# Kernel optimization log

Measured on AMD Instinct MI355X. Metric: run time of the kernel, lower is better.

Reference implementation:

```python
import jax, jax.numpy as jnp
import numpy as np

CHUNK = 64

def _l2norm(x, eps=1e-6):
    return x * jax.lax.rsqrt(jnp.sum(x * x, axis=-1, keepdims=True) + eps)

def _gated_delta_rule(query, key, value, g, beta, chunk_size=CHUNK):
    """Chunked gated delta-rule linear attention (Qwen3.5 GatedDeltaNet).
    query/key: [B,S,H,Dk], value: [B,S,H,Dv], g/beta: [B,S,H]. Returns [B,S,H,Dv]."""
    out_dtype = query.dtype
    # use_qk_l2norm_in_kernel=True
    query = _l2norm(query)
    key = _l2norm(key)
    # -> [B,H,S,D] fp32 (matches torch kernel's internal fp32 math)
    q, k, v = [jnp.transpose(x, (0, 2, 1, 3)).astype(jnp.float32) for x in (query, key, value)]
    gg, b = [jnp.transpose(x, (0, 2, 1)).astype(jnp.float32) for x in (g, beta)]
    B, H, S, Dk = k.shape
    Dv = v.shape[-1]
    C = chunk_size
    pad = (-S) % C  # static
    if pad:
        q = jnp.pad(q, ((0, 0), (0, 0), (0, pad), (0, 0)))
        k = jnp.pad(k, ((0, 0), (0, 0), (0, pad), (0, 0)))
        v = jnp.pad(v, ((0, 0), (0, 0), (0, pad), (0, 0)))
        gg = jnp.pad(gg, ((0, 0), (0, 0), (0, pad)))
        b = jnp.pad(b, ((0, 0), (0, 0), (0, pad)))
    Tlen = S + pad
    N = Tlen // C
    q = q * (Dk ** -0.5)
    v_beta = v * b[..., None]
    k_beta = k * b[..., None]
    rs = lambda x: x.reshape(B, H, N, C, x.shape[-1])
    q, k, v_beta, k_beta = map(rs, (q, k, v_beta, k_beta))
    gc = jnp.cumsum(gg.reshape(B, H, N, C), axis=-1)  # within-chunk cumulative log-decay
    tril = jnp.tril(jnp.ones((C, C), bool))
    strict = jnp.tril(jnp.ones((C, C), bool), -1)
    diff = gc[..., :, None] - gc[..., None, :]  # [B,H,N,C,C]
    decay = jnp.where(tril, jnp.exp(jnp.where(tril, diff, 0.0)), 0.0)
    # UT transform: torch's sequential row loop computes (I + strict_tril(k_beta k^T * decay))^{-1}
    M = jnp.where(strict, jnp.einsum('bhnck,bhndk->bhncd', k_beta, k) * decay, 0.0)
    eye = jnp.eye(C, dtype=jnp.float32)
    Tmat = jax.scipy.linalg.solve_triangular(eye + M, jnp.broadcast_to(eye, M.shape), lower=True)
    v_c = Tmat @ v_beta                                   # [B,H,N,C,Dv]
    k_cum = Tmat @ (k_beta * jnp.exp(gc)[..., None])      # [B,H,N,C,Dk]

    def step(state, inp):
        q_i, k_i, v_i, kc_i, dec_i, g_i = inp  # per-chunk [B,H,C,*]
        attn = jnp.einsum('bhck,bhdk->bhcd', q_i, k_i) * dec_i
        v_new = v_i - kc_i @ state
        out_i = (q_i * jnp.exp(g_i)[..., None]) @ state + attn @ v_new
        g_last = g_i[..., -1]
        kd = k_i * jnp.exp(g_last[..., None] - g_i)[..., None]
        state = state * jnp.exp(g_last)[..., None, None] + jnp.einsum('bhck,bhcv->bhkv', kd, v_new)
        return state, out_i

    mv = lambda x: jnp.moveaxis(x, 2, 0)  # chunk axis leading for scan
    init = jnp.zeros((B, H, Dk, Dv), jnp.float32)
    _, outs = jax.lax.scan(step, init, (mv(q), mv(k), mv(v_c), mv(k_cum), mv(decay), mv(gc)))
    out = jnp.moveaxis(outs, 0, 2).reshape(B, H, Tlen, Dv)[:, :, :S]
    return jnp.transpose(out, (0, 2, 1, 3)).astype(out_dtype)


def setup_inputs() -> dict:
    key = jax.random.key(0)
    ks = jax.random.split(key, 5)
    B, S, H, Dk, Dv = 2, 4096, 16, 128, 128
    q = jax.random.normal(ks[0], (B, S, H, Dk), jnp.float32)
    k = jax.random.normal(ks[1], (B, S, H, Dk), jnp.float32)
    v = jax.random.normal(ks[2], (B, S, H, Dv), jnp.float32)
    # g is log-decay, <= 0 (model computes g = -exp(A_log)*softplus(a + dt_bias))
    g = -jax.random.uniform(ks[3], (B, S, H), jnp.float32)
    beta = jax.random.uniform(ks[4], (B, S, H), jnp.float32)  # ~ sigmoid(b)
    return {"query": q, "key": k, "value": v, "g": g, "beta": beta}


def reference(query, key, value, g, beta):
    return _gated_delta_rule(query, key, value, g, beta)
```

## Files before the change

kernel.cpp:

```cpp
#include <hip/hip_runtime.h>
#include <math.h>


namespace {
constexpr int Bn = 2, Sn = 4096, Hn = 16, DKn = 128, DVn = 128, Cn = 64, Nn = 64;
constexpr int NBH = 32;
constexpr long CHUNK_B = 143360;
}

typedef __attribute__((ext_vector_type(4))) float f32x4;
typedef __attribute__((ext_vector_type(8))) _Float16 f16x8;
typedef __attribute__((ext_vector_type(4))) _Float16 f16x4;

__device__ __forceinline__ void fsplit(float x, _Float16& h, _Float16& l) {
  h = (_Float16)x;
  l = (_Float16)(x - (float)h);
}

__device__ __forceinline__ void gl_lds16(const void* g, void* l) {
  __builtin_amdgcn_global_load_lds(
      (const __attribute__((address_space(1))) void*)g,
      (__attribute__((address_space(3))) void*)l, 16, 0, 0);
}

#define MFMA16(D, A, B) D = __builtin_amdgcn_mfma_f32_16x16x32_f16(A, B, D, 0, 0, 0)

__device__ __forceinline__ int sidx(int r, int dk) {
  return r * 128 + (((dk >> 3) ^ (r & 7)) << 3) + (dk & 7);
}

__global__ __launch_bounds__(512, 1) void gdn_phaseA(
    const float* __restrict__ q, const float* __restrict__ k,
    const float* __restrict__ v, const float* __restrict__ g,
    const float* __restrict__ beta, char* __restrict__ wsb,
    int n0, int ncpp)
{
  __shared__ __align__(16) _Float16 sAh[8192], sAl[8192];
  __shared__ __align__(16) _Float16 sQh[8192], sQl[8192];
  __shared__ __align__(16) float sM[64][68];
  __shared__ __align__(16) float satt[4096];
  __shared__ __align__(16) float sV[64 * 132];
  __shared__ float s_gc[64], s_egc[64], s_inv[64], s_ekd[64], s_beta[64];

  const int t    = threadIdx.x;
  const int lane = t & 63;
  const int w    = t >> 6;
  const int pl  = blockIdx.x;
  const int bhx = pl / ncpp;
  const int nl  = pl % ncpp;
  const int n   = n0 + nl;
  const int hh_ = bhx % Hn;
  const int bb_ = bhx / Hn;
  const long base   = (((long)bb_ * Sn + (long)n * Cn) * Hn + hh_) * DKn;
  const long rowstr = (long)Hn * DKn;
  const long gbase  = ((long)bb_ * Sn + (long)n * Cn) * Hn + hh_;
  const long cb     = (long)pl * CHUNK_B;
  const long gloff  = (long)NBH * ncpp * CHUNK_B;

  #pragma unroll
  for (int i = 0; i < 4; ++i) {
    int idx = t + 512 * i;
    int r = idx >> 5, c4 = (idx & 31) << 2;
    *(f32x4*)&sV[r * 132 + c4] = *(const f32x4*)(v + base + (long)r * rowstr + c4);
  }

  if (t < 64) {
    s_beta[t] = beta[gbase + (long)t * Hn];
    float x = g[gbase + (long)t * Hn];
    #pragma unroll
    for (int s = 1; s < 64; s <<= 1) {
      float y = __shfl_up(x, s, 64);
      if (t >= s) x += y;
    }
    s_gc[t]  = x;
    float eg = expf(x);
    s_egc[t] = eg;
    s_inv[t] = expf(-x);
    float g63 = __shfl(x, 63, 64);
    s_ekd[t] = expf(g63 - x);
    if (t == 63) ((float*)(wsb + gloff))[pl] = eg;
  }

  {
    const int r = t >> 3, sub = t & 7;
    f32x4 ka[4], qa[4];
    #pragma unroll
    for (int i = 0; i < 4; ++i) {
      ka[i] = *(const f32x4*)(k + base + (long)r * rowstr + sub * 16 + 4 * i);
      qa[i] = *(const f32x4*)(q + base + (long)r * rowstr + sub * 16 + 4 * i);
    }
    float sk = 0.f, sq = 0.f;
    #pragma unroll
    for (int i = 0; i < 4; ++i) {
      sk += ka[i][0]*ka[i][0] + ka[i][1]*ka[i][1] + ka[i][2]*ka[i][2] + ka[i][3]*ka[i][3];
      sq += qa[i][0]*qa[i][0] + qa[i][1]*qa[i][1] + qa[i][2]*qa[i][2] + qa[i][3]*qa[i][3];
    }
    sk += __shfl_xor(sk, 1, 64); sk += __shfl_xor(sk, 2, 64); sk += __shfl_xor(sk, 4, 64);
    sq += __shfl_xor(sq, 1, 64); sq += __shfl_xor(sq, 2, 64); sq += __shfl_xor(sq, 4, 64);
    const float rk = rsqrtf(sk + 1e-6f);
    const float rq = rsqrtf(sq + 1e-6f) * 0.08838834764831845f;
    #pragma unroll
    for (int i = 0; i < 4; ++i) {
      const int dk0 = sub * 16 + 4 * i;
      const int go = sidx(r, dk0);
      f16x4 h4, l4, qh4, ql4;
      #pragma unroll
      for (int e = 0; e < 4; ++e) {
        _Float16 h_, l_;
        fsplit(ka[i][e] * rk, h_, l_); h4[e] = h_; l4[e] = l_;
        fsplit(qa[i][e] * rq, h_, l_); qh4[e] = h_; ql4[e] = l_;
      }
      *(f16x4*)&sAh[go] = h4;  *(f16x4*)&sAl[go] = l4;
      *(f16x4*)&sQh[go] = qh4; *(f16x4*)&sQl[go] = ql4;
    }
  }
  __syncthreads();

  {
    const int mt  = w & 3;
    const int tc0 = (w >> 2) * 2;
    const f32x4 zero = {0.f, 0.f, 0.f, 0.f};
    f32x4 mk0 = zero, mk1 = zero, ma0 = zero, ma1 = zero;
    #pragma unroll
    for (int kt = 0; kt < 4; ++kt) {
      const int rA = mt * 16 + (lane & 15);
      const int gA = rA * 128 + (((kt * 4 + (lane >> 4)) ^ (rA & 7)) << 3);
      f16x8 fa_h = *(const f16x8*)&sAh[gA];
      f16x8 fa_l = *(const f16x8*)&sAl[gA];
      #pragma unroll
      for (int j = 0; j < 2; ++j) {
        const int rB = (tc0 + j) * 16 + (lane & 15);
        const int gB = rB * 128 + (((kt * 4 + (lane >> 4)) ^ (rB & 7)) << 3);
        f16x8 fb_h = *(const f16x8*)&sAh[gB];
        f16x8 fb_l = *(const f16x8*)&sAl[gB];
        f16x8 fq_h = *(const f16x8*)&sQh[gB];
        f16x8 fq_l = *(const f16x8*)&sQl[gB];
        if (j == 0) {
          MFMA16(mk0, fa_h, fb_h); MFMA16(mk0, fa_h, fb_l); MFMA16(mk0, fa_l, fb_h);
          MFMA16(ma0, fa_h, fq_h); MFMA16(ma0, fa_h, fq_l); MFMA16(ma0, fa_l, fq_h);
        } else {
          MFMA16(mk1, fa_h, fb_h); MFMA16(mk1, fa_h, fb_l); MFMA16(mk1, fa_l, fb_h);
          MFMA16(ma1, fa_h, fq_h); MFMA16(ma1, fa_h, fq_l); MFMA16(ma1, fa_l, fq_h);
        }
      }
    }
    const int r0 = mt * 16 + (lane >> 4) * 4;
    #pragma unroll
    for (int j = 0; j < 2; ++j) {
      const int scol = (tc0 + j) * 16 + (lane & 15);
      const f32x4 mkv = (j == 0) ? mk0 : mk1;
      const f32x4 mav = (j == 0) ? ma0 : ma1;
      #pragma unroll
      for (int e = 0; e < 4; ++e) {
        const int r = r0 + e;
        sM[r][scol] = (r > scol) ? mkv[e] * s_beta[r] * s_egc[r] * s_inv[scol] : 0.f;
      }
      f32x4 av;
      #pragma unroll
      for (int e = 0; e < 4; ++e) {
        const int d = r0 + e;
        av[e] = (scol >= d) ? mav[e] * s_egc[scol] * s_inv[d] : 0.f;
      }
      *(f32x4*)&satt[scol * 64 + (((r0 >> 2) ^ (scol & 3)) << 2)] = av;
    }
  }
  __syncthreads();

  if (t < 256) {
    float X[64];
    const int j = t;
    if (j < 128) {
      #pragma unroll
      for (int i = 0; i < 64; ++i) {
        const int go = sidx(i, j);
        X[i] = ((float)sAh[go] + (float)sAl[go]) * s_beta[i] * s_egc[i];
      }
    } else {
      const int jj = j - 128;
      #pragma unroll
      for (int i = 0; i < 64; ++i)
        X[i] = sV[i * 132 + jj] * s_beta[i];
    }
    #pragma unroll
    for (int i = 1; i < 64; ++i) {
      float s0 = 0.f, s1 = 0.f, s2 = 0.f, s3 = 0.f;
      int l = 0;
      #pragma unroll
      for (; l + 4 <= i; l += 4) {
        f32x4 m = *(const f32x4*)&sM[i][l];
        s0 += m[0] * X[l];     s1 += m[1] * X[l + 1];
        s2 += m[2] * X[l + 2]; s3 += m[3] * X[l + 3];
      }
      float s = (s0 + s2) + (s1 + s3);
      #pragma unroll
      for (; l < i; ++l) s += sM[i][l] * X[l];
      X[i] -= s;
    }
    if (j < 128) {
      _Float16* KCh = (_Float16*)(wsb + cb);
      _Float16* KCl = (_Float16*)(wsb + cb + 16384);
      #pragma unroll
      for (int c = 0; c < 64; ++c) {
        const int tile = (c >> 4) * 4 + (j >> 5);
        const int ln_  = ((j >> 3) & 3) * 16 + (c & 15);
        const int o = tile * 512 + ln_ * 8 + (j & 7);
        _Float16 h_, l_; fsplit(X[c], h_, l_);
        KCh[o] = h_; KCl[o] = l_;
      }
    } else {
      float* VC = (float*)(wsb + cb + 110592);
      const int jj = j - 128;
      #pragma unroll
      for (int a = 0; a < 16; ++a) {
        f32x4 xx;
        xx[0] = X[4*a]; xx[1] = X[4*a+1]; xx[2] = X[4*a+2]; xx[3] = X[4*a+3];
        const int eo = ((jj >> 4) * 4 + (a >> 2)) * 256 + ((a & 3) * 16 + (jj & 15)) * 4;
        *(f32x4*)&VC[eo] = xx;
      }
    }
  } else {
    const int tt = t - 256;
    {
      _Float16* Hh = (_Float16*)(wsb + cb + 32768);
      _Float16* Ll = (_Float16*)(wsb + cb + 49152);
      #pragma unroll
      for (int i = 0; i < 8; ++i) {
        int o = i * 1024 + tt * 4;
        int tile = o >> 9, ln = (o >> 3) & 63;
        int row = (tile >> 2) * 16 + (ln & 15);
        int k0  = (tile & 3) * 32 + (ln >> 4) * 8 + (o & 7);
        const int go = sidx(row, k0);
        f16x4 qh4 = *(const f16x4*)&sQh[go];
        f16x4 ql4 = *(const f16x4*)&sQl[go];
        const float eg = s_egc[row];
        f16x4 hh, ll;
        #pragma unroll
        for (int r = 0; r < 4; ++r) {
          _Float16 h_, l_;
          fsplit(((float)qh4[r] + (float)ql4[r]) * eg, h_, l_);
          hh[r] = h_; ll[r] = l_;
        }
        *(f16x4*)(Hh + o) = hh; *(f16x4*)(Ll + o) = ll;
      }
    }
    {
      _Float16* Hh = (_Float16*)(wsb + cb + 65536);
      _Float16* Ll = (_Float16*)(wsb + cb + 81920);
      #pragma unroll
      for (int i = 0; i < 8; ++i) {
        int o = i * 1024 + tt * 4;
        int tile = o >> 9, ln = (o >> 3) & 63;
        int row = (tile >> 1) * 16 + (ln & 15);
        int k0  = (tile & 1) * 32 + (ln >> 4) * 8 + (o & 7);
        f16x4 hh, ll;
        #pragma unroll
        for (int r = 0; r < 4; ++r) {
          const int c = k0 + r;
          const int go = sidx(c, row);
          _Float16 h_, l_;
          fsplit(((float)sAh[go] + (float)sAl[go]) * s_ekd[c], h_, l_);
          hh[r] = h_; ll[r] = l_;
        }
        *(f16x4*)(Hh + o) = hh; *(f16x4*)(Ll + o) = ll;
      }
    }
    {
      _Float16* Hh = (_Float16*)(wsb + cb + 98304);
      _Float16* Ll = (_Float16*)(wsb + cb + 104448);
      #pragma unroll
      for (int i = 0; i < 3; ++i) {
        int o = i * 1024 + tt * 4;
        int s = o >> 9, ln = (o >> 3) & 63;
        int mt  = (s < 4) ? s : (s - 2);
        int kt2 = (s < 4) ? 0 : 1;
        int row = mt * 16 + (ln & 15);
        int k0  = kt2 * 32 + (ln >> 4) * 8 + (o & 7);
        f32x4 av = *(const f32x4*)&satt[row * 64 + ((((k0 >> 2) ^ (row & 3))) << 2)];
        f16x4 hh, ll;
        #pragma unroll
        for (int r = 0; r < 4; ++r) {
          _Float16 h_, l_; fsplit(av[r], h_, l_);
          hh[r] = h_; ll[r] = l_;
        }
        *(f16x4*)(Hh + o) = hh; *(f16x4*)(Ll + o) = ll;
      }
    }
  }
}

#define VMW(N) do { asm volatile("s_waitcnt vmcnt(" #N ")" ::: "memory"); \
                    __builtin_amdgcn_sched_barrier(0); } while (0)
#define BAR() do { __builtin_amdgcn_s_barrier(); \
                   __builtin_amdgcn_sched_barrier(0); } while (0)

#define STAGEW2(dst, srcB, nt) do {                                   \
    const char* s_ = (const char*)(srcB);                             \
    char* d_ = (char*)(dst);                                          \
    _Pragma("unroll")                                                 \
    for (int t_ = wave; t_ < (nt); t_ += 2)                           \
      gl_lds16(s_ + t_ * 1024 + lane * 16, d_ + t_ * 1024 + lane * 16); \
  } while (0)

__global__ __launch_bounds__(128, 1) void gdn_phaseB(
    char* __restrict__ wsb, float* __restrict__ out,
    int n0, int ncpp, int lastpass)
{
  __shared__ __align__(16) _Float16 sKCh[8192], sKCl[8192];
  __shared__ __align__(16) _Float16 sQGh[8192], sQGl[8192];
  __shared__ __align__(16) _Float16 sKDh[8192], sKDl[8192];
  __shared__ __align__(16) _Float16 sAT[6144];
  __shared__ __align__(16) _Float16 Sb[2][2][16][128];
  __shared__ __align__(16) _Float16 Ub[2][2][16][64];

  const int tid  = threadIdx.x;
  const int wave = tid >> 6;
  const int lane = tid & 63;
  const int jrow = lane & 15;
  const int kgrp = lane >> 4;
  const int jx3  = (jrow & 7) << 3;

  const int blk    = blockIdx.x;
  const int bhl    = blk & 31;
  const int sharer = blk >> 5;
  const int jb     = sharer * 2 + wave;
  const int h   = bhl % Hn;
  const int b   = bhl / Hn;
  const long gloff = (long)NBH * ncpp * CHUNK_B;
  const float* GLp = (const float*)(wsb + gloff);
  float* STp = (float*)(wsb + gloff + 32768) + (((long)bhl * 8 + jb) * 64 + lane) * 32;
  const char* cbase = wsb + (long)bhl * ncpp * CHUNK_B;

  f32x4 S[8];
  const f32x4 zero = {0.f, 0.f, 0.f, 0.f};
  if (n0 == 0) {
    #pragma unroll
    for (int i = 0; i < 8; ++i) S[i] = zero;
  } else {
    #pragma unroll
    for (int i = 0; i < 8; ++i) S[i] = *(const f32x4*)(STp + i * 4);
  }
  #pragma unroll
  for (int dt = 0; dt < 8; ++dt) {
    f16x4 hh, ll; _Float16 h_, l_;
    #pragma unroll
    for (int r = 0; r < 4; ++r) { fsplit(S[dt][r], h_, l_); hh[r] = h_; ll[r] = l_; }
    const int cx = (dt * 16 + kgrp * 4) ^ jx3;
    *(f16x4*)&Sb[wave][0][jrow][cx] = hh;
    *(f16x4*)&Sb[wave][1][jrow][cx] = ll;
  }

  f32x4 vcv[4];
  {
    const float* VC0 = (const float*)(cbase + 110592);
    #pragma unroll
    for (int ct = 0; ct < 4; ++ct)
      vcv[ct] = *(const f32x4*)(VC0 + ((jb * 4 + ct) * 64 + lane) * 4);
  }
  float glc = GLp[(long)bhl * ncpp];
  STAGEW2(sKCh, cbase +     0, 16); STAGEW2(sKCl, cbase + 16384, 16);
  STAGEW2(sQGh, cbase + 32768, 16); STAGEW2(sQGl, cbase + 49152, 16);
  STAGEW2(sAT,  cbase + 98304, 12);
  asm volatile("s_waitcnt vmcnt(0) lgkmcnt(0)" ::: "memory");
  __builtin_amdgcn_sched_barrier(0);
  BAR();

  float* outb = out + ((long)b * Sn) * (long)(Hn * DVn) + (long)h * DVn + jb * 16 + jrow;

  #pragma unroll 1
  for (int nl = 0; nl < ncpp; ++nl) {
    const int  np  = (nl + 1 < ncpp) ? nl + 1 : nl;
    const char* cbp = cbase + (long)nl * CHUNK_B;
    const char* cbn = cbase + (long)np * CHUNK_B;
    const int n = n0 + nl;

    VMW(38); BAR();
    STAGEW2(sKDh, cbp + 65536, 16); STAGEW2(sKDl, cbp + 81920, 16);
    f32x4 vcvN[4];
    {
      const float* VCn = (const float*)(cbn + 110592);
      #pragma unroll
      for (int ct = 0; ct < 4; ++ct)
        vcvN[ct] = *(const f32x4*)(VCn + ((jb * 4 + ct) * 64 + lane) * 4);
    }
    const float glN = GLp[(long)bhl * ncpp + np];

    f16x8 sbh[4], sbl[4];
    #pragma unroll
    for (int kt = 0; kt < 4; ++kt) {
      const int cx = (kt * 32 + kgrp * 8) ^ jx3;
      sbh[kt] = *(const f16x8*)&Sb[wave][0][jrow][cx];
      sbl[kt] = *(const f16x8*)&Sb[wave][1][jrow][cx];
    }
    f32x4 aA[4], aB[4], aC[4];
    #pragma unroll
    for (int i = 0; i < 4; ++i) { aA[i] = zero; aB[i] = zero; aC[i] = zero; }
    #pragma unroll
    for (int kt = 0; kt < 4; ++kt) {
      #pragma unroll
      for (int mt = 0; mt < 4; ++mt) {
        const int tl = mt * 4 + kt;
        f16x8 ah = *(const f16x8*)&sKCh[tl * 512 + lane * 8];
        f16x8 al = *(const f16x8*)&sKCl[tl * 512 + lane * 8];
        MFMA16(aA[mt], ah, sbh[kt]);
        MFMA16(aB[mt], ah, sbl[kt]);
        MFMA16(aC[mt], al, sbh[kt]);
      }
    }
    #pragma unroll
    for (int ct = 0; ct < 4; ++ct) {
      f32x4 uu = vcv[ct] - (aA[ct] + aB[ct] + aC[ct]);
      f16x4 hh, ll; _Float16 h_, l_;
      #pragma unroll
      for (int r = 0; r < 4; ++r) { fsplit(uu[r], h_, l_); hh[r] = h_; ll[r] = l_; }
      const int cu = (ct * 16 + kgrp * 4) ^ jx3;
      *(f16x4*)&Ub[wave][0][jrow][cu] = hh;
      *(f16x4*)&Ub[wave][1][jrow][cu] = ll;
    }

    VMW(42); BAR();
    STAGEW2(sKCh, cbn +     0, 16); STAGEW2(sKCl, cbn + 16384, 16);

    f32x4 oA[4], oB[4], oC[4];
    #pragma unroll
    for (int i = 0; i < 4; ++i) { oA[i] = zero; oB[i] = zero; oC[i] = zero; }
    #pragma unroll
    for (int kt = 0; kt < 4; ++kt) {
      #pragma unroll
      for (int mt = 0; mt < 4; ++mt) {
        const int tl = mt * 4 + kt;
        f16x8 ah = *(const f16x8*)&sQGh[tl * 512 + lane * 8];
        f16x8 al = *(const f16x8*)&sQGl[tl * 512 + lane * 8];
        MFMA16(oA[mt], ah, sbh[kt]);
        MFMA16(oB[mt], ah, sbl[kt]);
        MFMA16(oC[mt], al, sbh[kt]);
      }
    }

    VMW(52); BAR();
    STAGEW2(sQGh, cbn + 32768, 16); STAGEW2(sQGl, cbn + 49152, 16);

    f16x8 ubh[2], ubl[2];
    #pragma unroll
    for (int kt2 = 0; kt2 < 2; ++kt2) {
      const int cx = (kt2 * 32 + kgrp * 8) ^ jx3;
      ubh[kt2] = *(const f16x8*)&Ub[wave][0][jrow][cx];
      ubl[kt2] = *(const f16x8*)&Ub[wave][1][jrow][cx];
    }
    #pragma unroll
    for (int kt2 = 0; kt2 < 2; ++kt2) {
      #pragma unroll
      for (int mt = 0; mt < 4; ++mt) {
        if (kt2 == 1 && mt < 2) continue;
        const int slot = (kt2 == 0) ? mt : (mt + 2);
        f16x8 ah = *(const f16x8*)&sAT[slot * 512 + lane * 8];
        f16x8 al = *(const f16x8*)&sAT[3072 + slot * 512 + lane * 8];
        MFMA16(oA[mt], ah, ubh[kt2]);
        MFMA16(oB[mt], ah, ubl[kt2]);
        MFMA16(oC[mt], al, ubh[kt2]);
      }
    }

    VMW(36); BAR();
    STAGEW2(sAT, cbn + 98304, 12);

    #pragma unroll
    for (int i = 0; i < 8; ++i) {
      S[i][0] *= glc; S[i][1] *= glc; S[i][2] *= glc; S[i][3] *= glc;
    }
    #pragma unroll
    for (int kt2 = 0; kt2 < 2; ++kt2) {
      #pragma unroll
      for (int dt = 0; dt < 8; ++dt) {
        const int tl = dt * 2 + kt2;
        f16x8 ah = *(const f16x8*)&sKDh[tl * 512 + lane * 8];
        f16x8 al = *(const f16x8*)&sKDl[tl * 512 + lane * 8];
        MFMA16(S[dt], ah, ubh[kt2]);
        MFMA16(S[dt], ah, ubl[kt2]);
        MFMA16(S[dt], al, ubh[kt2]);
      }
    }
    #pragma unroll
    for (int dt = 0; dt < 8; ++dt) {
      f16x4 hh, ll; _Float16 h_, l_;
      #pragma unroll
      for (int r = 0; r < 4; ++r) { fsplit(S[dt][r], h_, l_); hh[r] = h_; ll[r] = l_; }
      const int cx = (dt * 16 + kgrp * 4) ^ jx3;
      *(f16x4*)&Sb[wave][0][jrow][cx] = hh;
      *(f16x4*)&Sb[wave][1][jrow][cx] = ll;
    }

    {
      float* orow = outb + (long)(n * 64) * (Hn * DVn);
      #pragma unroll
      for (int ct = 0; ct < 4; ++ct) {
        f32x4 o4 = oA[ct] + oB[ct] + oC[ct];
        #pragma unroll
        for (int r = 0; r < 4; ++r)
          orow[(long)(ct * 16 + kgrp * 4 + r) * (Hn * DVn)] = o4[r];
      }
    }

    #pragma unroll
    for (int ct = 0; ct < 4; ++ct) vcv[ct] = vcvN[ct];
    glc = glN;
  }

  if (!lastpass) {
    #pragma unroll
    for (int i = 0; i < 8; ++i) *(f32x4*)(STp + i * 4) = S[i];
  }
}

extern "C" void kernel_launch(void* const* d_in, const int* in_sizes, int n_in,
                              void* d_out, int out_size, void* d_ws, size_t ws_size,
                              hipStream_t stream) {
  (void)in_sizes; (void)n_in; (void)out_size;
  const float* q    = (const float*)d_in[0];
  const float* k    = (const float*)d_in[1];
  const float* v    = (const float*)d_in[2];
  const float* g    = (const float*)d_in[3];
  const float* beta = (const float*)d_in[4];
  char*  ws  = (char*)d_ws;
  float* out = (float*)d_out;

  int NCP = 8;
  for (int c = 64; c >= 8; c >>= 1) {
    long need = (long)NBH * c * CHUNK_B + 32768 + 2097152;
    if ((size_t)need <= ws_size) { NCP = c; break; }
  }

  for (int n0 = 0; n0 < Nn; n0 += NCP) {
    const int last = (n0 + NCP >= Nn) ? 1 : 0;
    hipLaunchKernelGGL(gdn_phaseA, dim3(NBH * NCP), dim3(512), 0, stream,
                       q, k, v, g, beta, ws, n0, NCP);
    hipLaunchKernelGGL(gdn_phaseB, dim3(128), dim3(128), 0, stream,
                       ws, out, n0, NCP, last);
  }
}
```

Measured before the change: 451.8 us.

## Merge phaseB MFMA stages, restage loads, move scattered output stores to epilogue kernel

```diff
diff --git a/kernel.cpp b/kernel.cpp
--- a/kernel.cpp
+++ b/kernel.cpp
@@ -302,8 +302,7 @@
   } while (0)
 
 __global__ __launch_bounds__(128, 1) void gdn_phaseB(
-    char* __restrict__ wsb, float* __restrict__ out,
-    int n0, int ncpp, int lastpass)
+    char* __restrict__ wsb, int n0, int ncpp, int lastpass)
 {
   __shared__ __align__(16) _Float16 sKCh[8192], sKCl[8192];
   __shared__ __align__(16) _Float16 sQGh[8192], sQGl[8192];
@@ -323,11 +322,10 @@
   const int bhl    = blk & 31;
   const int sharer = blk >> 5;
   const int jb     = sharer * 2 + wave;
-  const int h   = bhl % Hn;
-  const int b   = bhl / Hn;
   const long gloff = (long)NBH * ncpp * CHUNK_B;
   const float* GLp = (const float*)(wsb + gloff);
   float* STp = (float*)(wsb + gloff + 32768) + (((long)bhl * 8 + jb) * 64 + lane) * 32;
+  float* outw = (float*)(wsb + gloff + 32768 + 2097152);
   const char* cbase = wsb + (long)bhl * ncpp * CHUNK_B;
 
   f32x4 S[8];
@@ -359,22 +357,19 @@
   float glc = GLp[(long)bhl * ncpp];
   STAGEW2(sKCh, cbase +     0, 16); STAGEW2(sKCl, cbase + 16384, 16);
   STAGEW2(sQGh, cbase + 32768, 16); STAGEW2(sQGl, cbase + 49152, 16);
-  STAGEW2(sAT,  cbase + 98304, 12);
   asm volatile("s_waitcnt vmcnt(0) lgkmcnt(0)" ::: "memory");
   __builtin_amdgcn_sched_barrier(0);
   BAR();
-
-  float* outb = out + ((long)b * Sn) * (long)(Hn * DVn) + (long)h * DVn + jb * 16 + jrow;
 
   #pragma unroll 1
   for (int nl = 0; nl < ncpp; ++nl) {
     const int  np  = (nl + 1 < ncpp) ? nl + 1 : nl;
     const char* cbp = cbase + (long)nl * CHUNK_B;
     const char* cbn = cbase + (long)np * CHUNK_B;
-    const int n = n0 + nl;
-
-    VMW(38); BAR();
+
+    VMW(4); BAR();
     STAGEW2(sKDh, cbp + 65536, 16); STAGEW2(sKDl, cbp + 81920, 16);
+    STAGEW2(sAT,  cbp + 98304, 12);
     f32x4 vcvN[4];
     {
       const float* VCn = (const float*)(cbn + 110592);
@@ -391,9 +386,12 @@
       sbh[kt] = *(const f16x8*)&Sb[wave][0][jrow][cx];
       sbl[kt] = *(const f16x8*)&Sb[wave][1][jrow][cx];
     }
-    f32x4 aA[4], aB[4], aC[4];
-    #pragma unroll
-    for (int i = 0; i < 4; ++i) { aA[i] = zero; aB[i] = zero; aC[i] = zero; }
+    f32x4 aA[4], aB[4], aC[4], oA[4], oB[4], oC[4];
+    #pragma unroll
+    for (int i = 0; i < 4; ++i) {
+      aA[i] = zero; aB[i] = zero; aC[i] = zero;
+      oA[i] = zero; oB[i] = zero; oC[i] = zero;
+    }
     #pragma unroll
     for (int kt = 0; kt < 4; ++kt) {
       #pragma unroll
@@ -404,6 +402,11 @@
         MFMA16(aA[mt], ah, sbh[kt]);
         MFMA16(aB[mt], ah, sbl[kt]);
         MFMA16(aC[mt], al, sbh[kt]);
+        f16x8 qh = *(const f16x8*)&sQGh[tl * 512 + lane * 8];
+        f16x8 ql = *(const f16x8*)&sQGl[tl * 512 + lane * 8];
+        MFMA16(oA[mt], qh, sbh[kt]);
+        MFMA16(oB[mt], qh, sbl[kt]);
+        MFMA16(oC[mt], ql, sbh[kt]);
       }
     }
     #pragma unroll
@@ -416,29 +419,6 @@
       *(f16x4*)&Ub[wave][0][jrow][cu] = hh;
       *(f16x4*)&Ub[wave][1][jrow][cu] = ll;
     }
-
-    VMW(42); BAR();
-    STAGEW2(sKCh, cbn +     0, 16); STAGEW2(sKCl, cbn + 16384, 16);
-
-    f32x4 oA[4], oB[4], oC[4];
-    #pragma unroll
-    for (int i = 0; i < 4; ++i) { oA[i] = zero; oB[i] = zero; oC[i] = zero; }
-    #pragma unroll
-    for (int kt = 0; kt < 4; ++kt) {
-      #pragma unroll
-      for (int mt = 0; mt < 4; ++mt) {
-        const int tl = mt * 4 + kt;
-        f16x8 ah = *(const f16x8*)&sQGh[tl * 512 + lane * 8];
-        f16x8 al = *(const f16x8*)&sQGl[tl * 512 + lane * 8];
-        MFMA16(oA[mt], ah, sbh[kt]);
-        MFMA16(oB[mt], ah, sbl[kt]);
-        MFMA16(oC[mt], al, sbh[kt]);
-      }
-    }
-
-    VMW(52); BAR();
-    STAGEW2(sQGh, cbn + 32768, 16); STAGEW2(sQGl, cbn + 49152, 16);
-
     f16x8 ubh[2], ubl[2];
     #pragma unroll
     for (int kt2 = 0; kt2 < 2; ++kt2) {
@@ -446,6 +426,11 @@
       ubh[kt2] = *(const f16x8*)&Ub[wave][0][jrow][cx];
       ubl[kt2] = *(const f16x8*)&Ub[wave][1][jrow][cx];
     }
+
+    VMW(4); BAR();
+    STAGEW2(sKCh, cbn +     0, 16); STAGEW2(sKCl, cbn + 16384, 16);
+    STAGEW2(sQGh, cbn + 32768, 16); STAGEW2(sQGl, cbn + 49152, 16);
+
     #pragma unroll
     for (int kt2 = 0; kt2 < 2; ++kt2) {
       #pragma unroll
@@ -459,10 +444,14 @@
         MFMA16(oC[mt], al, ubh[kt2]);
       }
     }
-
-    VMW(36); BAR();
-    STAGEW2(sAT, cbn + 98304, 12);
-
+    {
+      float* slab = outw + ((long)(bhl * ncpp + nl) * 8192) + jb * 1024;
+      #pragma unroll
+      for (int ct = 0; ct < 4; ++ct) {
+        f32x4 o4 = oA[ct] + oB[ct] + oC[ct];
+        *(f32x4*)(slab + (ct * 64 + lane) * 4) = o4;
+      }
+    }
     #pragma unroll
     for (int i = 0; i < 8; ++i) {
       S[i][0] *= glc; S[i][1] *= glc; S[i][2] *= glc; S[i][3] *= glc;
@@ -489,17 +478,6 @@
       *(f16x4*)&Sb[wave][1][jrow][cx] = ll;
     }
 
-    {
-      float* orow = outb + (long)(n * 64) * (Hn * DVn);
-      #pragma unroll
-      for (int ct = 0; ct < 4; ++ct) {
-        f32x4 o4 = oA[ct] + oB[ct] + oC[ct];
-        #pragma unroll
-        for (int r = 0; r < 4; ++r)
-          orow[(long)(ct * 16 + kgrp * 4 + r) * (Hn * DVn)] = o4[r];
-      }
-    }
-
     #pragma unroll
     for (int ct = 0; ct < 4; ++ct) vcv[ct] = vcvN[ct];
     glc = glN;
@@ -508,6 +486,42 @@
   if (!lastpass) {
     #pragma unroll
     for (int i = 0; i < 8; ++i) *(f32x4*)(STp + i * 4) = S[i];
+  }
+}
+
+__global__ __launch_bounds__(256, 1) void gdn_epi(
+    const char* __restrict__ wsb, float* __restrict__ out,
+    int n0, int ncpp)
+{
+  __shared__ float sT[64][132];
+  const int t   = threadIdx.x;
+  const int pl  = blockIdx.x;
+  const int bhl = pl / ncpp;
+  const int nl  = pl % ncpp;
+  const int n   = n0 + nl;
+  const int h   = bhl % Hn;
+  const int b   = bhl / Hn;
+  const long gloff = (long)NBH * ncpp * CHUNK_B;
+  const float* slab = (const float*)(wsb + gloff + 32768 + 2097152) + (long)pl * 8192;
+
+  #pragma unroll
+  for (int i = 0; i < 8; ++i) {
+    int idx = t + 256 * i;
+    int o = idx * 4;
+    int jb = o >> 10, ct = (o >> 8) & 3, ln = (o >> 2) & 63;
+    int row = ct * 16 + (ln >> 4) * 4;
+    int col = jb * 16 + (ln & 15);
+    f32x4 v = *(const f32x4*)(slab + o);
+    sT[row + 0][col] = v[0]; sT[row + 1][col] = v[1];
+    sT[row + 2][col] = v[2]; sT[row + 3][col] = v[3];
+  }
+  __syncthreads();
+  const long obase = (((long)b * Sn + (long)n * 64) * Hn + h) * DVn;
+  #pragma unroll
+  for (int i = 0; i < 8; ++i) {
+    int idx = t + 256 * i;
+    int r2 = idx >> 5, c4 = (idx & 31) << 2;
+    *(f32x4*)(out + obase + (long)r2 * (Hn * DVn) + c4) = *(const f32x4*)&sT[r2][c4];
   }
 }
 
@@ -525,7 +539,8 @@
 
   int NCP = 8;
   for (int c = 64; c >= 8; c >>= 1) {
-    long need = (long)NBH * c * CHUNK_B + 32768 + 2097152;
+    long need = (long)NBH * c * CHUNK_B + 32768 + 2097152
+              + (long)NBH * c * 32768;
     if ((size_t)need <= ws_size) { NCP = c; break; }
   }
 
@@ -534,6 +549,8 @@
     hipLaunchKernelGGL(gdn_phaseA, dim3(NBH * NCP), dim3(512), 0, stream,
                        q, k, v, g, beta, ws, n0, NCP);
     hipLaunchKernelGGL(gdn_phaseB, dim3(128), dim3(128), 0, stream,
-                       ws, out, n0, NCP, last);
-  }
-}
+                       ws, n0, NCP, last);
+    hipLaunchKernelGGL(gdn_epi, dim3(NBH * NCP), dim3(256), 0, stream,
+                       ws, out, n0, NCP);
+  }
+}
```

New measurement: 467.3 us. 3.4% more time.
